# Performance work log

Measured on AMD Instinct MI355X. Metric: run time of the kernel, lower is better.

The kernel has to match this reference:

```python
import jax, jax.numpy as jnp
import numpy as np

B, N, C = 16, 2048, 10
PARAMS = [128, 128, 128, 64]
K = 16


def setup_inputs() -> dict:
    key = jax.random.key(0)
    ks = jax.random.split(key, 1 + 3 * len(PARAMS))
    inp = {"x": jax.random.normal(ks[0], (B, N, C), dtype=jnp.float32)}
    last = C
    i = 1
    for li, p in enumerate(PARAMS):
        s = 1.0 / np.sqrt(last)  # torch Linear default init range
        inp[f"w_rel_{li}"] = jax.random.uniform(ks[i], (last, p), jnp.float32, -s, s); i += 1
        inp[f"w_root_{li}"] = jax.random.uniform(ks[i], (last, p), jnp.float32, -s, s); i += 1
        inp[f"b_{li}"] = jax.random.uniform(ks[i], (p,), jnp.float32, -s, s); i += 1
        last = p
    inp["k"] = K
    return inp


def _knn_edge_index(x, k):
    # kNN per batch element, excluding self; equivalent to
    # topk(norm(x_i - x_j), k+1, largest=False)[:, :, 1:] in the torch code.
    b, n, _ = x.shape
    x2 = jnp.sum(x * x, axis=-1)                          # [b,n]
    d2 = x2[:, :, None] + x2[:, None, :] - 2.0 * jnp.einsum('bic,bjc->bij', x, x)
    d2 = d2.at[:, jnp.arange(n), jnp.arange(n)].set(jnp.inf)  # drop self
    nbors = jax.lax.top_k(-d2, k)[1]                      # [b,n,k] nearest indices
    off = (jnp.arange(b) * n)[:, None, None]              # batch offset into flat nodes
    src = jnp.broadcast_to(jnp.arange(n)[None, :, None] + off, (b, n, k)).reshape(-1)
    dst = (nbors + off).reshape(-1)
    return src, dst


def reference(x, w_rel_0, w_root_0, b_0, w_rel_1, w_root_1, b_1,
              w_rel_2, w_root_2, b_2, w_rel_3, w_root_3, b_3, k):
    b, n, c = x.shape
    k = min(k, n - 1)
    src, dst = _knn_edge_index(x, k)
    layers = [(w_rel_0, w_root_0, b_0), (w_rel_1, w_root_1, b_1),
              (w_rel_2, w_root_2, b_2), (w_rel_3, w_root_3, b_3)]
    h = x.reshape(b * n, c)
    for li, (wr, wo, bb) in enumerate(layers):
        # PyG GraphConv: out = lin_rel(sum_{(u,v) in E} x_u) + lin_root(x_v)
        agg = jax.ops.segment_sum(h[src], dst, num_segments=b * n)  # scatter-add at dst
        h = agg @ wr + bb + h @ wo
        if li < len(layers) - 1:
            h = jax.nn.relu(h)
    h = h.reshape(b, n, -1)
    edge_vals = jnp.einsum('bic,bjc->bij', h, h)  # final bilinear score [b,n,n]
    return edge_vals[:, None]                     # [b,1,n,n]
```

## Files before the change

kernel.cpp:

```cpp
#include <hip/hip_runtime.h>
#include <math.h>

#define BB_   16
#define NN_   2048
#define CDIM  10
#define KNN   16
#define NNODES (BB_*NN_)
#define NEDGES (NNODES*KNN)

__global__ __launch_bounds__(256) void prep_kernel(const float* __restrict__ x,
                                                   float* __restrict__ x2,
                                                   float* __restrict__ xt,
                                                   int* __restrict__ indeg) {
    int g = blockIdx.x * 256 + threadIdx.x;
    if (g >= NNODES) return;
    const int bb = g >> 11;
    const int j  = g & (NN_ - 1);
    const float* xr = x + (size_t)g * CDIM;
    float* xtb = xt + (size_t)bb * CDIM * NN_;
    float s = 0.f;
#pragma unroll
    for (int c = 0; c < CDIM; ++c) {
        float v = xr[c];
        s = fmaf(v, v, s);
        xtb[c * NN_ + j] = v;
    }
    x2[g] = s;
    indeg[g] = 0;
}

__device__ __forceinline__ unsigned fkey(float f) {
    unsigned u = __float_as_uint(f);
    return ((int)u >= 0) ? (u ^ 0x80000000u) : ~u;
}

__device__ __forceinline__ void bitonic64(unsigned& hi, unsigned& lo, int lane) {
#pragma unroll
    for (int k = 2; k <= 64; k <<= 1) {
#pragma unroll
        for (int j = k >> 1; j > 0; j >>= 1) {
            unsigned ohi = __shfl_xor(hi, j, 64);
            unsigned olo = __shfl_xor(lo, j, 64);
            bool up    = ((lane & k) == 0);
            bool lower = ((lane & j) == 0);
            bool oless = (ohi < hi) || (ohi == hi && olo < lo);
            bool take  = (lower == up) ? oless : !oless;
            hi = take ? ohi : hi;
            lo = take ? olo : lo;
        }
    }
}

__device__ __forceinline__ unsigned slot_to_jj(int slot, int lane) {
    return (unsigned)(((slot >> 4) << 10) + (((slot >> 2) & 3) << 8) + (lane << 2) + (slot & 3));
}

__global__ __launch_bounds__(512) void knn_kernel(const float* __restrict__ x,
                                                  const float* __restrict__ xt,
                                                  const float* __restrict__ x2,
                                                  int* __restrict__ nbors,
                                                  int* __restrict__ indeg) {
    __shared__ __align__(16) float s_pl[11 * 1024];
    __shared__ unsigned s_hi[8][64];
    __shared__ unsigned s_lo[8][64];
    const int wv   = threadIdx.x >> 6;
    const int lane = threadIdx.x & 63;
    const int g  = blockIdx.x * 8 + wv;
    const int bb = g >> 11;
    const int il = g & (NN_ - 1);

    float xp[CDIM];
    const float* xr = x + (size_t)g * CDIM;
#pragma unroll
    for (int c = 0; c < CDIM; ++c) xp[c] = xr[c];

    const float* xtb = xt + (size_t)bb * CDIM * NN_;
    const float* x2b = x2 + bb * NN_;
    const float4* s_pl4 = (const float4*)s_pl;

    unsigned ud[32];
    unsigned min_hi = 0xFFFFFFFFu, min_lo = 0xFFFFFFFFu;

    for (int tile = 0; tile < 2; ++tile) {
        const int tb = tile << 10;
        __syncthreads();
        {
            const int t0 = threadIdx.x;
#pragma unroll
            for (int r = 0; r < 22; ++r) {
                const int idx = r * 512 + t0;
                const int c = idx >> 10;
                const int j = idx & 1023;
                s_pl[idx] = (c < 10) ? xtb[c * NN_ + tb + j] : x2b[tb + j];
            }
        }
        __syncthreads();
#pragma unroll
        for (int it = 0; it < 4; ++it) {
            const int fo = it * 64 + lane;
            float4 dot = {0.f, 0.f, 0.f, 0.f};
#pragma unroll
            for (int c = 0; c < CDIM; ++c) {
                float4 v = s_pl4[c * 256 + fo];
                dot.x = fmaf(xp[c], v.x, dot.x);
                dot.y = fmaf(xp[c], v.y, dot.y);
                dot.z = fmaf(xp[c], v.z, dot.z);
                dot.w = fmaf(xp[c], v.w, dot.w);
            }
            const float4 xn = s_pl4[10 * 256 + fo];
            float kd[4];
            kd[0] = xn.x - 2.f * dot.x;
            kd[1] = xn.y - 2.f * dot.y;
            kd[2] = xn.z - 2.f * dot.z;
            kd[3] = xn.w - 2.f * dot.w;
            const int jbase = tb + it * 256 + (lane << 2);
#pragma unroll
            for (int q = 0; q < 4; ++q) {
                const int jj = jbase + q;
                unsigned u = fkey(kd[q]);
                if (jj == il) u = 0xFFFFFFFFu;
                ud[tile * 16 + it * 4 + q] = u;
                bool less = (u < min_hi) || (u == min_hi && (unsigned)jj < min_lo);
                min_hi = less ? u : min_hi;
                min_lo = less ? (unsigned)jj : min_lo;
            }
        }
    }

    unsigned bh = min_hi, bl = min_lo;
    bitonic64(bh, bl, lane);
    const unsigned m_hi = __shfl(bh, 15, 64);
    const unsigned m_lo = __shfl(bl, 15, 64);

    int c = 0;
#pragma unroll
    for (int slot = 0; slot < 32; ++slot) {
        const unsigned jj = slot_to_jj(slot, lane);
        const unsigned u  = ud[slot];
        bool q = (u < m_hi) || (u == m_hi && jj <= m_lo);
        c += q ? 1 : 0;
    }
    int pos = c;
#pragma unroll
    for (int m = 1; m < 64; m <<= 1) {
        int o = __shfl_up(pos, m, 64);
        if (lane >= m) pos += o;
    }
    const int total = __shfl(pos, 63, 64);
    pos -= c;

    if (total <= 64) {
#pragma unroll
        for (int slot = 0; slot < 32; ++slot) {
            const unsigned jj = slot_to_jj(slot, lane);
            const unsigned u  = ud[slot];
            bool q = (u < m_hi) || (u == m_hi && jj <= m_lo);
            if (q) { s_hi[wv][pos] = u; s_lo[wv][pos] = jj; pos++; }
        }
        unsigned u2 = (lane < total) ? s_hi[wv][lane] : 0xFFFFFFFFu;
        unsigned l2 = (lane < total) ? s_lo[wv][lane] : (0x80000000u + (unsigned)lane);
        bitonic64(u2, l2, lane);
        if (lane < KNN) {
            const int jglob = bb * NN_ + (int)l2;
            nbors[(size_t)g * KNN + lane] = jglob;
            atomicAdd(&indeg[jglob], 1);
        }
    } else {
        unsigned taken = 0;
        for (int r = 0; r < KNN; ++r) {
            unsigned b_hi = 0xFFFFFFFFu, b_lo = 0xFFFFFFFFu;
#pragma unroll
            for (int slot = 0; slot < 32; ++slot) {
                const unsigned jj = slot_to_jj(slot, lane);
                const unsigned u  = ud[slot];
                bool avail = ((taken >> slot) & 1u) == 0u;
                bool less  = avail && ((u < b_hi) || (u == b_hi && jj < b_lo));
                b_hi = less ? u : b_hi;
                b_lo = less ? jj : b_lo;
            }
            unsigned w_hi = b_hi, w_lo = b_lo;
#pragma unroll
            for (int m = 32; m >= 1; m >>= 1) {
                unsigned oh = __shfl_xor(w_hi, m, 64);
                unsigned ol = __shfl_xor(w_lo, m, 64);
                bool less = (oh < w_hi) || (oh == w_hi && ol < w_lo);
                w_hi = less ? oh : w_hi;
                w_lo = less ? ol : w_lo;
            }
            if (b_hi == w_hi && b_lo == w_lo) {
                const int ws = ((int)(b_lo >> 10) << 4) + (((int)(b_lo >> 8) & 3) << 2) + (int)(b_lo & 3);
                taken |= 1u << ws;
                const int jglob = bb * NN_ + (int)w_lo;
                nbors[(size_t)g * KNN + r] = jglob;
                atomicAdd(&indeg[jglob], 1);
            }
        }
    }
}

__global__ __launch_bounds__(1024) void scan_kernel(const int* __restrict__ indeg,
                                                    int* __restrict__ offs,
                                                    int* __restrict__ cursor) {
    __shared__ int part[1024];
    int t = threadIdx.x;
    int4 lv[8];
    int s = 0;
#pragma unroll
    for (int i = 0; i < 8; ++i) {
        lv[i] = ((const int4*)indeg)[t * 8 + i];
        s += lv[i].x + lv[i].y + lv[i].z + lv[i].w;
    }
    part[t] = s;
    __syncthreads();
    for (int d = 1; d < 1024; d <<= 1) {
        int add = (t >= d) ? part[t - d] : 0;
        __syncthreads();
        part[t] += add;
        __syncthreads();
    }
    int run = part[t] - s;
#pragma unroll
    for (int i = 0; i < 8; ++i) {
        int4 o;
        o.x = run; run += lv[i].x;
        o.y = run; run += lv[i].y;
        o.z = run; run += lv[i].z;
        o.w = run; run += lv[i].w;
        ((int4*)offs)[t * 8 + i]   = o;
        ((int4*)cursor)[t * 8 + i] = o;
    }
    if (t == 1023) offs[NNODES] = run;
}

__global__ __launch_bounds__(256) void fill_kernel(const int* __restrict__ nbors,
                                                   int* __restrict__ cursor,
                                                   int* __restrict__ rev) {
    int e = blockIdx.x * 256 + threadIdx.x;
    if (e >= NEDGES) return;
    int dst = nbors[e];
    int src = e >> 4;
    int pos = atomicAdd(&cursor[dst], 1);
    rev[pos] = src;
}

template<int CIN, int COUT, int GS, bool RELU>
__global__ __launch_bounds__(256) void layer_kernel(const float* __restrict__ in,
                                                    const float* __restrict__ wrel,
                                                    const float* __restrict__ wroot,
                                                    const float* __restrict__ bias,
                                                    const int* __restrict__ offs,
                                                    const int* __restrict__ rev,
                                                    float* __restrict__ out) {
    constexpr int NT = 8;
    __shared__ float s_ai[NT][CIN][2];
    const int j0 = blockIdx.x * NT;
    const int t  = threadIdx.x;

    constexpr int NG = 256 / GS;
    const int grp = t / GS, cc = t % GS;
    for (int nt = grp; nt < NT; nt += NG) {
        const int j = j0 + nt;
        if (cc < CIN) s_ai[nt][cc][1] = in[(size_t)j * CIN + cc];
        float agg = 0.f;
        const int e0 = offs[j], e1 = offs[j + 1];
        for (int e = e0; e < e1; ++e) {
            const int s = rev[e];
            if (cc < CIN) agg += in[(size_t)s * CIN + cc];
        }
        if (cc < CIN) s_ai[nt][cc][0] = agg;
    }
    __syncthreads();

    constexpr int REP = 256 / COUT;
    constexpr int NPT = NT / REP;
    const int c = t % COUT, r = t / COUT;
    float acc[NPT];
#pragma unroll
    for (int u = 0; u < NPT; ++u) acc[u] = bias[c];
#pragma unroll 4
    for (int k = 0; k < CIN; ++k) {
        const float wrv = wrel[k * COUT + c];
        const float wov = wroot[k * COUT + c];
#pragma unroll
        for (int u = 0; u < NPT; ++u) {
            const int nt = r + u * REP;
            acc[u] = fmaf(s_ai[nt][k][0], wrv, acc[u]);
            acc[u] = fmaf(s_ai[nt][k][1], wov, acc[u]);
        }
    }
#pragma unroll
    for (int u = 0; u < NPT; ++u) {
        const int nt = r + u * REP;
        float v = acc[u];
        if (RELU) v = fmaxf(v, 0.f);
        out[(size_t)(j0 + nt) * COUT + c] = v;
    }
}

template<int COUT, bool RELU>
__global__ __launch_bounds__(256) void layer_big_kernel(const float* __restrict__ in,
                                                        const float* __restrict__ wrel,
                                                        const float* __restrict__ wroot,
                                                        const float* __restrict__ bias,
                                                        const int* __restrict__ offs,
                                                        const int* __restrict__ rev,
                                                        float* __restrict__ out) {
    constexpr int CIN = 128;
    constexpr int NT  = 64;
    __shared__ float s_agg[NT][CIN];
    __shared__ float s_own[NT][CIN];
    const int j0 = blockIdx.x * NT;
    const int t  = threadIdx.x;

    {
        const int ng  = t >> 5;
        const int c4  = (t & 31) * 4;
#pragma unroll
        for (int r = 0; r < NT / 8; ++r) {
            const int nt = r * 8 + ng;
            const int j  = j0 + nt;
            float4 own = *(const float4*)(in + (size_t)j * CIN + c4);
            float4 a0 = {0.f,0.f,0.f,0.f}, a1 = a0, a2 = a0, a3 = a0;
            const int e0 = offs[j], e1 = offs[j + 1];
            int e = e0;
            for (; e + 4 <= e1; e += 4) {
                const int s0 = rev[e], s1 = rev[e+1], s2 = rev[e+2], s3 = rev[e+3];
                float4 v0 = *(const float4*)(in + (size_t)s0 * CIN + c4);
                float4 v1 = *(const float4*)(in + (size_t)s1 * CIN + c4);
                float4 v2 = *(const float4*)(in + (size_t)s2 * CIN + c4);
                float4 v3 = *(const float4*)(in + (size_t)s3 * CIN + c4);
                a0.x += v0.x; a0.y += v0.y; a0.z += v0.z; a0.w += v0.w;
                a1.x += v1.x; a1.y += v1.y; a1.z += v1.z; a1.w += v1.w;
                a2.x += v2.x; a2.y += v2.y; a2.z += v2.z; a2.w += v2.w;
                a3.x += v3.x; a3.y += v3.y; a3.z += v3.z; a3.w += v3.w;
            }
            for (; e < e1; ++e) {
                const int s0 = rev[e];
                float4 v0 = *(const float4*)(in + (size_t)s0 * CIN + c4);
                a0.x += v0.x; a0.y += v0.y; a0.z += v0.z; a0.w += v0.w;
            }
            float4 agg;
            agg.x = (a0.x + a1.x) + (a2.x + a3.x);
            agg.y = (a0.y + a1.y) + (a2.y + a3.y);
            agg.z = (a0.z + a1.z) + (a2.z + a3.z);
            agg.w = (a0.w + a1.w) + (a2.w + a3.w);
            *(float4*)(&s_agg[nt][c4]) = agg;
            *(float4*)(&s_own[nt][c4]) = own;
        }
    }
    __syncthreads();

    constexpr int CG  = COUT / 4;
    constexpr int NGG = 256 / CG;
    constexpr int NPN = NT / NGG;
    const int cg = t % CG, ng2 = t / CG;
    const int c4 = cg * 4;
    const int nb = ng2 * NPN;

    float acc[NPN][4];
    {
        const float4 b4 = *(const float4*)(bias + c4);
#pragma unroll
        for (int u = 0; u < NPN; ++u) {
            acc[u][0] = b4.x; acc[u][1] = b4.y; acc[u][2] = b4.z; acc[u][3] = b4.w;
        }
    }

#pragma unroll 2
    for (int k4 = 0; k4 < CIN; k4 += 4) {
        float4 wr_[4], wo_[4];
#pragma unroll
        for (int kk = 0; kk < 4; ++kk) {
            wr_[kk] = *(const float4*)(wrel  + (size_t)(k4 + kk) * COUT + c4);
            wo_[kk] = *(const float4*)(wroot + (size_t)(k4 + kk) * COUT + c4);
        }
#pragma unroll
        for (int u = 0; u < NPN; ++u) {
            const int n = nb + u;
            float4 ag = *(const float4*)(&s_agg[n][k4]);
            float4 ow = *(const float4*)(&s_own[n][k4]);
            acc[u][0] = fmaf(ag.x, wr_[0].x, acc[u][0]); acc[u][0] = fmaf(ag.y, wr_[1].x, acc[u][0]);
            acc[u][0] = fmaf(ag.z, wr_[2].x, acc[u][0]); acc[u][0] = fmaf(ag.w, wr_[3].x, acc[u][0]);
            acc[u][0] = fmaf(ow.x, wo_[0].x, acc[u][0]); acc[u][0] = fmaf(ow.y, wo_[1].x, acc[u][0]);
            acc[u][0] = fmaf(ow.z, wo_[2].x, acc[u][0]); acc[u][0] = fmaf(ow.w, wo_[3].x, acc[u][0]);

            acc[u][1] = fmaf(ag.x, wr_[0].y, acc[u][1]); acc[u][1] = fmaf(ag.y, wr_[1].y, acc[u][1]);
            acc[u][1] = fmaf(ag.z, wr_[2].y, acc[u][1]); acc[u][1] = fmaf(ag.w, wr_[3].y, acc[u][1]);
            acc[u][1] = fmaf(ow.x, wo_[0].y, acc[u][1]); acc[u][1] = fmaf(ow.y, wo_[1].y, acc[u][1]);
            acc[u][1] = fmaf(ow.z, wo_[2].y, acc[u][1]); acc[u][1] = fmaf(ow.w, wo_[3].y, acc[u][1]);

            acc[u][2] = fmaf(ag.x, wr_[0].z, acc[u][2]); acc[u][2] = fmaf(ag.y, wr_[1].z, acc[u][2]);
            acc[u][2] = fmaf(ag.z, wr_[2].z, acc[u][2]); acc[u][2] = fmaf(ag.w, wr_[3].z, acc[u][2]);
            acc[u][2] = fmaf(ow.x, wo_[0].z, acc[u][2]); acc[u][2] = fmaf(ow.y, wo_[1].z, acc[u][2]);
            acc[u][2] = fmaf(ow.z, wo_[2].z, acc[u][2]); acc[u][2] = fmaf(ow.w, wo_[3].z, acc[u][2]);

            acc[u][3] = fmaf(ag.x, wr_[0].w, acc[u][3]); acc[u][3] = fmaf(ag.y, wr_[1].w, acc[u][3]);
            acc[u][3] = fmaf(ag.z, wr_[2].w, acc[u][3]); acc[u][3] = fmaf(ag.w, wr_[3].w, acc[u][3]);
            acc[u][3] = fmaf(ow.x, wo_[0].w, acc[u][3]); acc[u][3] = fmaf(ow.y, wo_[1].w, acc[u][3]);
            acc[u][3] = fmaf(ow.z, wo_[2].w, acc[u][3]); acc[u][3] = fmaf(ow.w, wo_[3].w, acc[u][3]);
        }
    }

#pragma unroll
    for (int u = 0; u < NPN; ++u) {
        const int j = j0 + nb + u;
        float4 v;
        v.x = acc[u][0]; v.y = acc[u][1]; v.z = acc[u][2]; v.w = acc[u][3];
        if (RELU) {
            v.x = fmaxf(v.x, 0.f); v.y = fmaxf(v.y, 0.f);
            v.z = fmaxf(v.z, 0.f); v.w = fmaxf(v.w, 0.f);
        }
        *(float4*)(out + (size_t)j * COUT + c4) = v;
    }
}

#define EIDX(j) ((j) + ((j) >> 5))
__global__ __launch_bounds__(256) void edge_kernel(const float* __restrict__ h,
                                                   float* __restrict__ out) {
    __shared__ float tI[32][132];
    __shared__ float tJ[32][132];
    const int b = blockIdx.y;
    int rem = blockIdx.x;
    int bi = 0;
    while (rem >= 16 - bi) { rem -= 16 - bi; ++bi; }
    const int bj = bi + rem;
    const int i0 = bi * 128;
    const int j0 = bj * 128;
    const float* hb = h + (size_t)b * NN_ * 64;
    const int t = threadIdx.x;

    float acc[8][8];
#pragma unroll
    for (int u = 0; u < 8; ++u)
#pragma unroll
        for (int v = 0; v < 8; ++v) acc[u][v] = 0.f;

    const int ti = (t >> 4) * 8;
    const int tj = (t & 15) * 8;
    const int sr = t >> 1;
    const int sg = (t & 1) * 16;

    for (int kc = 0; kc < 2; ++kc) {
        if (kc) __syncthreads();
        {
            const float* srcI = hb + (size_t)(i0 + sr) * 64 + kc * 32 + sg;
            const float* srcJ = hb + (size_t)(j0 + sr) * 64 + kc * 32 + sg;
            const int ri = EIDX(sr);
#pragma unroll
            for (int v = 0; v < 4; ++v) {
                float4 fi = *(const float4*)(srcI + v * 4);
                float4 fj = *(const float4*)(srcJ + v * 4);
                const int c = sg + v * 4;
                tI[c + 0][ri] = fi.x; tI[c + 1][ri] = fi.y;
                tI[c + 2][ri] = fi.z; tI[c + 3][ri] = fi.w;
                tJ[c + 0][ri] = fj.x; tJ[c + 1][ri] = fj.y;
                tJ[c + 2][ri] = fj.z; tJ[c + 3][ri] = fj.w;
            }
        }
        __syncthreads();

        const int ia = EIDX(ti), ja = EIDX(tj);
#pragma unroll 4
        for (int k = 0; k < 32; ++k) {
            float4 a0 = *(const float4*)(&tI[k][ia]);
            float4 a1 = *(const float4*)(&tI[k][ia + 4]);
            float4 b0 = *(const float4*)(&tJ[k][ja]);
            float4 b1 = *(const float4*)(&tJ[k][ja + 4]);
            float av[8] = {a0.x, a0.y, a0.z, a0.w, a1.x, a1.y, a1.z, a1.w};
            float bv[8] = {b0.x, b0.y, b0.z, b0.w, b1.x, b1.y, b1.z, b1.w};
#pragma unroll
            for (int u = 0; u < 8; ++u)
#pragma unroll
                for (int v = 0; v < 8; ++v) acc[u][v] = fmaf(av[u], bv[v], acc[u][v]);
        }
    }

#pragma unroll
    for (int u = 0; u < 8; ++u) {
        float* dst = out + ((size_t)b * NN_ + (i0 + ti + u)) * NN_ + (j0 + tj);
        float4 w0; w0.x = acc[u][0]; w0.y = acc[u][1]; w0.z = acc[u][2]; w0.w = acc[u][3];
        float4 w1; w1.x = acc[u][4]; w1.y = acc[u][5]; w1.z = acc[u][6]; w1.w = acc[u][7];
        *(float4*)(dst)     = w0;
        *(float4*)(dst + 4) = w1;
    }

    if (bi != bj) {
#pragma unroll
        for (int v = 0; v < 8; ++v) {
            float* dstm = out + ((size_t)b * NN_ + (j0 + tj + v)) * NN_ + (i0 + ti);
            float4 m0; m0.x = acc[0][v]; m0.y = acc[1][v]; m0.z = acc[2][v]; m0.w = acc[3][v];
            float4 m1; m1.x = acc[4][v]; m1.y = acc[5][v]; m1.z = acc[6][v]; m1.w = acc[7][v];
            *(float4*)(dstm)     = m0;
            *(float4*)(dstm + 4) = m1;
        }
    }
}

extern "C" void kernel_launch(void* const* d_in, const int* in_sizes, int n_in,
                              void* d_out, int out_size, void* d_ws, size_t ws_size,
                              hipStream_t stream) {
    (void)in_sizes; (void)n_in; (void)out_size; (void)ws_size;
    const float* x = (const float*)d_in[0];
    const float* wr[4] = {(const float*)d_in[1],  (const float*)d_in[4],
                          (const float*)d_in[7],  (const float*)d_in[10]};
    const float* wo[4] = {(const float*)d_in[2],  (const float*)d_in[5],
                          (const float*)d_in[8],  (const float*)d_in[11]};
    const float* bs[4] = {(const float*)d_in[3],  (const float*)d_in[6],
                          (const float*)d_in[9],  (const float*)d_in[12]};
    float* out = (float*)d_out;

    char* w = (char*)d_ws;
    size_t o = 0;
    auto alloc = [&](size_t bytes) { void* p = w + o; o = (o + bytes + 255) & ~(size_t)255; return p; };
    int*   nbors  = (int*)  alloc((size_t)NEDGES * 4);
    int*   indeg  = (int*)  alloc((size_t)NNODES * 4);
    int*   offs   = (int*)  alloc((size_t)(NNODES + 1) * 4);
    int*   cursor = (int*)  alloc((size_t)NNODES * 4);
    int*   rev    = (int*)  alloc((size_t)NEDGES * 4);
    float* x2     = (float*)alloc((size_t)NNODES * 4);
    float* xt     = (float*)alloc((size_t)NNODES * CDIM * 4);
    float* hA     = (float*)alloc((size_t)NNODES * 128 * 4);
    float* hB     = (float*)alloc((size_t)NNODES * 128 * 4);

    prep_kernel<<<NNODES / 256, 256, 0, stream>>>(x, x2, xt, indeg);
    knn_kernel<<<NNODES / 8, 512, 0, stream>>>(x, xt, x2, nbors, indeg);
    scan_kernel<<<1, 1024, 0, stream>>>(indeg, offs, cursor);
    fill_kernel<<<NEDGES / 256, 256, 0, stream>>>(nbors, cursor, rev);

    layer_kernel<CDIM, 128, 16, true ><<<NNODES / 8, 256, 0, stream>>>(x,  wr[0], wo[0], bs[0], offs, rev, hA);
    layer_big_kernel<128, true ><<<NNODES / 64, 256, 0, stream>>>(hA, wr[1], wo[1], bs[1], offs, rev, hB);
    layer_big_kernel<128, true ><<<NNODES / 64, 256, 0, stream>>>(hB, wr[2], wo[2], bs[2], offs, rev, hA);
    layer_big_kernel<64,  false><<<NNODES / 64, 256, 0, stream>>>(hA, wr[3], wo[3], bs[3], offs, rev, hB);

    edge_kernel<<<dim3(136, 16, 1), 256, 0, stream>>>(hB, out);
}
```

Before: 741.2 us.

## Process two query rows per wave in kNN and shrink layer tiles

The kNN kernel now has each wave compute distances for two query points against each shared-memory tile. This halves the shared-memory loads per distance and halves the block size to 256 threads, with the selection logic factored into a helper. The layer_big kernel tile shrinks from 64 to 32 nodes to launch more blocks, its gather loop gains an 8-way unrolled stage, and the GEMM loop unroll rises to 4. Costs are higher register pressure from the doubled ud arrays and each block reloading the full tile for fewer threads.

```diff
diff --git a/kernel.cpp b/kernel.cpp
--- a/kernel.cpp
+++ b/kernel.cpp
@@ -55,78 +55,12 @@
     return (unsigned)(((slot >> 4) << 10) + (((slot >> 2) & 3) << 8) + (lane << 2) + (slot & 3));
 }
 
-__global__ __launch_bounds__(512) void knn_kernel(const float* __restrict__ x,
-                                                  const float* __restrict__ xt,
-                                                  const float* __restrict__ x2,
-                                                  int* __restrict__ nbors,
-                                                  int* __restrict__ indeg) {
-    __shared__ __align__(16) float s_pl[11 * 1024];
-    __shared__ unsigned s_hi[8][64];
-    __shared__ unsigned s_lo[8][64];
-    const int wv   = threadIdx.x >> 6;
-    const int lane = threadIdx.x & 63;
-    const int g  = blockIdx.x * 8 + wv;
-    const int bb = g >> 11;
-    const int il = g & (NN_ - 1);
-
-    float xp[CDIM];
-    const float* xr = x + (size_t)g * CDIM;
-#pragma unroll
-    for (int c = 0; c < CDIM; ++c) xp[c] = xr[c];
-
-    const float* xtb = xt + (size_t)bb * CDIM * NN_;
-    const float* x2b = x2 + bb * NN_;
-    const float4* s_pl4 = (const float4*)s_pl;
-
-    unsigned ud[32];
-    unsigned min_hi = 0xFFFFFFFFu, min_lo = 0xFFFFFFFFu;
-
-    for (int tile = 0; tile < 2; ++tile) {
-        const int tb = tile << 10;
-        __syncthreads();
-        {
-            const int t0 = threadIdx.x;
-#pragma unroll
-            for (int r = 0; r < 22; ++r) {
-                const int idx = r * 512 + t0;
-                const int c = idx >> 10;
-                const int j = idx & 1023;
-                s_pl[idx] = (c < 10) ? xtb[c * NN_ + tb + j] : x2b[tb + j];
-            }
-        }
-        __syncthreads();
-#pragma unroll
-        for (int it = 0; it < 4; ++it) {
-            const int fo = it * 64 + lane;
-            float4 dot = {0.f, 0.f, 0.f, 0.f};
-#pragma unroll
-            for (int c = 0; c < CDIM; ++c) {
-                float4 v = s_pl4[c * 256 + fo];
-                dot.x = fmaf(xp[c], v.x, dot.x);
-                dot.y = fmaf(xp[c], v.y, dot.y);
-                dot.z = fmaf(xp[c], v.z, dot.z);
-                dot.w = fmaf(xp[c], v.w, dot.w);
-            }
-            const float4 xn = s_pl4[10 * 256 + fo];
-            float kd[4];
-            kd[0] = xn.x - 2.f * dot.x;
-            kd[1] = xn.y - 2.f * dot.y;
-            kd[2] = xn.z - 2.f * dot.z;
-            kd[3] = xn.w - 2.f * dot.w;
-            const int jbase = tb + it * 256 + (lane << 2);
-#pragma unroll
-            for (int q = 0; q < 4; ++q) {
-                const int jj = jbase + q;
-                unsigned u = fkey(kd[q]);
-                if (jj == il) u = 0xFFFFFFFFu;
-                ud[tile * 16 + it * 4 + q] = u;
-                bool less = (u < min_hi) || (u == min_hi && (unsigned)jj < min_lo);
-                min_hi = less ? u : min_hi;
-                min_lo = less ? (unsigned)jj : min_lo;
-            }
-        }
-    }
-
+__device__ __forceinline__ void select_row(const unsigned (&ud)[32],
+                                           unsigned min_hi, unsigned min_lo,
+                                           int lane, int g, int bb,
+                                           unsigned (&sh)[64], unsigned (&sl)[64],
+                                           int* __restrict__ nbors,
+                                           int* __restrict__ indeg) {
     unsigned bh = min_hi, bl = min_lo;
     bitonic64(bh, bl, lane);
     const unsigned m_hi = __shfl(bh, 15, 64);
@@ -155,10 +89,10 @@
             const unsigned jj = slot_to_jj(slot, lane);
             const unsigned u  = ud[slot];
             bool q = (u < m_hi) || (u == m_hi && jj <= m_lo);
-            if (q) { s_hi[wv][pos] = u; s_lo[wv][pos] = jj; pos++; }
-        }
-        unsigned u2 = (lane < total) ? s_hi[wv][lane] : 0xFFFFFFFFu;
-        unsigned l2 = (lane < total) ? s_lo[wv][lane] : (0x80000000u + (unsigned)lane);
+            if (q) { sh[pos] = u; sl[pos] = jj; pos++; }
+        }
+        unsigned u2 = (lane < total) ? sh[lane] : 0xFFFFFFFFu;
+        unsigned l2 = (lane < total) ? sl[lane] : (0x80000000u + (unsigned)lane);
         bitonic64(u2, l2, lane);
         if (lane < KNN) {
             const int jglob = bb * NN_ + (int)l2;
@@ -196,6 +130,92 @@
             }
         }
     }
+}
+
+__global__ __launch_bounds__(256) void knn_kernel(const float* __restrict__ x,
+                                                  const float* __restrict__ xt,
+                                                  const float* __restrict__ x2,
+                                                  int* __restrict__ nbors,
+                                                  int* __restrict__ indeg) {
+    __shared__ __align__(16) float s_pl[11 * 1024];
+    __shared__ unsigned s_hi[4][64];
+    __shared__ unsigned s_lo[4][64];
+    const int wv   = threadIdx.x >> 6;
+    const int lane = threadIdx.x & 63;
+    const int g0 = blockIdx.x * 8 + wv * 2;
+    const int bb  = g0 >> 11;
+    const int il0 = g0 & (NN_ - 1);
+    const int il1 = il0 + 1;
+
+    float xpa[CDIM], xpb[CDIM];
+    const float* xra = x + (size_t)g0 * CDIM;
+#pragma unroll
+    for (int c = 0; c < CDIM; ++c) { xpa[c] = xra[c]; xpb[c] = xra[CDIM + c]; }
+
+    const float* xtb = xt + (size_t)bb * CDIM * NN_;
+    const float* x2b = x2 + bb * NN_;
+    const float4* s_pl4 = (const float4*)s_pl;
+
+    unsigned uda[32], udb[32];
+    unsigned mina_hi = 0xFFFFFFFFu, mina_lo = 0xFFFFFFFFu;
+    unsigned minb_hi = 0xFFFFFFFFu, minb_lo = 0xFFFFFFFFu;
+
+    for (int tile = 0; tile < 2; ++tile) {
+        const int tb = tile << 10;
+        __syncthreads();
+        {
+            const int t0 = threadIdx.x;
+#pragma unroll 4
+            for (int r = 0; r < 44; ++r) {
+                const int idx = r * 256 + t0;
+                const int c = idx >> 10;
+                const int j = idx & 1023;
+                s_pl[idx] = (c < 10) ? xtb[c * NN_ + tb + j] : x2b[tb + j];
+            }
+        }
+        __syncthreads();
+#pragma unroll
+        for (int it = 0; it < 4; ++it) {
+            const int fo = it * 64 + lane;
+            float4 da = {0.f, 0.f, 0.f, 0.f};
+            float4 db = {0.f, 0.f, 0.f, 0.f};
+#pragma unroll
+            for (int c = 0; c < CDIM; ++c) {
+                float4 v = s_pl4[c * 256 + fo];
+                da.x = fmaf(xpa[c], v.x, da.x); da.y = fmaf(xpa[c], v.y, da.y);
+                da.z = fmaf(xpa[c], v.z, da.z); da.w = fmaf(xpa[c], v.w, da.w);
+                db.x = fmaf(xpb[c], v.x, db.x); db.y = fmaf(xpb[c], v.y, db.y);
+                db.z = fmaf(xpb[c], v.z, db.z); db.w = fmaf(xpb[c], v.w, db.w);
+            }
+            const float4 xn = s_pl4[10 * 256 + fo];
+            float ka[4], kb[4];
+            ka[0] = xn.x - 2.f * da.x; ka[1] = xn.y - 2.f * da.y;
+            ka[2] = xn.z - 2.f * da.z; ka[3] = xn.w - 2.f * da.w;
+            kb[0] = xn.x - 2.f * db.x; kb[1] = xn.y - 2.f * db.y;
+            kb[2] = xn.z - 2.f * db.z; kb[3] = xn.w - 2.f * db.w;
+            const int jbase = tb + it * 256 + (lane << 2);
+#pragma unroll
+            for (int q = 0; q < 4; ++q) {
+                const int jj = jbase + q;
+                unsigned ua = fkey(ka[q]);
+                unsigned ub = fkey(kb[q]);
+                if (jj == il0) ua = 0xFFFFFFFFu;
+                if (jj == il1) ub = 0xFFFFFFFFu;
+                const int slot = tile * 16 + it * 4 + q;
+                uda[slot] = ua;
+                udb[slot] = ub;
+                bool la = (ua < mina_hi) || (ua == mina_hi && (unsigned)jj < mina_lo);
+                mina_hi = la ? ua : mina_hi;
+                mina_lo = la ? (unsigned)jj : mina_lo;
+                bool lb = (ub < minb_hi) || (ub == minb_hi && (unsigned)jj < minb_lo);
+                minb_hi = lb ? ub : minb_hi;
+                minb_lo = lb ? (unsigned)jj : minb_lo;
+            }
+        }
+    }
+
+    select_row(uda, mina_hi, mina_lo, lane, g0,     bb, s_hi[wv], s_lo[wv], nbors, indeg);
+    select_row(udb, minb_hi, minb_lo, lane, g0 + 1, bb, s_hi[wv], s_lo[wv], nbors, indeg);
 }
 
 __global__ __launch_bounds__(1024) void scan_kernel(const int* __restrict__ indeg,
@@ -306,7 +326,7 @@
                                                         const int* __restrict__ rev,
                                                         float* __restrict__ out) {
     constexpr int CIN = 128;
-    constexpr int NT  = 64;
+    constexpr int NT  = 32;
     __shared__ float s_agg[NT][CIN];
     __shared__ float s_own[NT][CIN];
     const int j0 = blockIdx.x * NT;
@@ -323,6 +343,26 @@
             float4 a0 = {0.f,0.f,0.f,0.f}, a1 = a0, a2 = a0, a3 = a0;
             const int e0 = offs[j], e1 = offs[j + 1];
             int e = e0;
+            for (; e + 8 <= e1; e += 8) {
+                const int s0 = rev[e],   s1 = rev[e+1], s2 = rev[e+2], s3 = rev[e+3];
+                const int s4 = rev[e+4], s5 = rev[e+5], s6 = rev[e+6], s7 = rev[e+7];
+                float4 v0 = *(const float4*)(in + (size_t)s0 * CIN + c4);
+                float4 v1 = *(const float4*)(in + (size_t)s1 * CIN + c4);
+                float4 v2 = *(const float4*)(in + (size_t)s2 * CIN + c4);
+                float4 v3 = *(const float4*)(in + (size_t)s3 * CIN + c4);
+                float4 v4 = *(const float4*)(in + (size_t)s4 * CIN + c4);
+                float4 v5 = *(const float4*)(in + (size_t)s5 * CIN + c4);
+                float4 v6 = *(const float4*)(in + (size_t)s6 * CIN + c4);
+                float4 v7 = *(const float4*)(in + (size_t)s7 * CIN + c4);
+                a0.x += v0.x; a0.y += v0.y; a0.z += v0.z; a0.w += v0.w;
+                a1.x += v1.x; a1.y += v1.y; a1.z += v1.z; a1.w += v1.w;
+                a2.x += v2.x; a2.y += v2.y; a2.z += v2.z; a2.w += v2.w;
+                a3.x += v3.x; a3.y += v3.y; a3.z += v3.z; a3.w += v3.w;
+                a0.x += v4.x; a0.y += v4.y; a0.z += v4.z; a0.w += v4.w;
+                a1.x += v5.x; a1.y += v5.y; a1.z += v5.z; a1.w += v5.w;
+                a2.x += v6.x; a2.y += v6.y; a2.z += v6.z; a2.w += v6.w;
+                a3.x += v7.x; a3.y += v7.y; a3.z += v7.z; a3.w += v7.w;
+            }
             for (; e + 4 <= e1; e += 4) {
                 const int s0 = rev[e], s1 = rev[e+1], s2 = rev[e+2], s3 = rev[e+3];
                 float4 v0 = *(const float4*)(in + (size_t)s0 * CIN + c4);
@@ -366,7 +406,7 @@
         }
     }
 
-#pragma unroll 2
+#pragma unroll 4
     for (int k4 = 0; k4 < CIN; k4 += 4) {
         float4 wr_[4], wo_[4];
 #pragma unroll
@@ -523,14 +563,14 @@
     float* hB     = (float*)alloc((size_t)NNODES * 128 * 4);
 
     prep_kernel<<<NNODES / 256, 256, 0, stream>>>(x, x2, xt, indeg);
-    knn_kernel<<<NNODES / 8, 512, 0, stream>>>(x, xt, x2, nbors, indeg);
+    knn_kernel<<<NNODES / 8, 256, 0, stream>>>(x, xt, x2, nbors, indeg);
     scan_kernel<<<1, 1024, 0, stream>>>(indeg, offs, cursor);
     fill_kernel<<<NEDGES / 256, 256, 0, stream>>>(nbors, cursor, rev);
 
     layer_kernel<CDIM, 128, 16, true ><<<NNODES / 8, 256, 0, stream>>>(x,  wr[0], wo[0], bs[0], offs, rev, hA);
-    layer_big_kernel<128, true ><<<NNODES / 64, 256, 0, stream>>>(hA, wr[1], wo[1], bs[1], offs, rev, hB);
-    layer_big_kernel<128, true ><<<NNODES / 64, 256, 0, stream>>>(hB, wr[2], wo[2], bs[2], offs, rev, hA);
-    layer_big_kernel<64,  false><<<NNODES / 64, 256, 0, stream>>>(hA, wr[3], wo[3], bs[3], offs, rev, hB);
+    layer_big_kernel<128, true ><<<NNODES / 32, 256, 0, stream>>>(hA, wr[1], wo[1], bs[1], offs, rev, hB);
+    layer_big_kernel<128, true ><<<NNODES / 32, 256, 0, stream>>>(hB, wr[2], wo[2], bs[2], offs, rev, hA);
+    layer_big_kernel<64,  false><<<NNODES / 32, 256, 0, stream>>>(hA, wr[3], wo[3], bs[3], offs, rev, hB);
 
     edge_kernel<<<dim3(136, 16, 1), 256, 0, stream>>>(hB, out);
 }
```

New measurement: 810.9 us. 1.09x slower.
